# Performance work log

Hardware: AMD Instinct MI355X
Metric: run time of the kernel (lower is better)

## Reference

```python
import jax, jax.numpy as jnp
import numpy as np

U_COUNT = 100000
I_COUNT = 50000
DIM = 64
N_EDGES = 3200000
BATCH = 16384


def setup_inputs() -> dict:
    key = jax.random.key(0)
    ks = jax.random.split(key, 8)
    user_emb = jax.random.normal(ks[0], (U_COUNT, DIM), dtype=jnp.float32) * 0.01
    item_emb = jax.random.normal(ks[1], (I_COUNT, DIM), dtype=jnp.float32) * 0.01
    edge_vals = jax.random.uniform(ks[2], (N_EDGES,), dtype=jnp.float32)
    edge_user = jax.random.randint(ks[3], (N_EDGES,), 0, U_COUNT, dtype=jnp.int32)
    edge_item = jax.random.randint(ks[4], (N_EDGES,), 0, I_COUNT, dtype=jnp.int32)
    user = jax.random.randint(ks[5], (BATCH,), 0, U_COUNT, dtype=jnp.int32)
    pos_item = jax.random.randint(ks[6], (BATCH,), 0, I_COUNT, dtype=jnp.int32)
    neg_item = jax.random.randint(ks[7], (BATCH,), 0, I_COUNT, dtype=jnp.int32)
    return {"user_emb": user_emb, "item_emb": item_emb, "edge_vals": edge_vals,
            "edge_user": edge_user, "edge_item": edge_item,
            "user": user, "pos_item": pos_item, "neg_item": neg_item}


def reference(user_emb, item_emb, edge_vals, edge_user, edge_item, user, pos_item, neg_item):
    # A is the [U, I] normalized adjacency in COO form (edge_user, edge_item, edge_vals).
    # u = A @ x_items : gather item rows, scale, scatter-add into user segments.
    def spmm_A(x_items):  # [I, D] -> [U, D]
        msgs = edge_vals[:, None] * x_items[edge_item]  # [E, D]
        return jax.ops.segment_sum(msgs, edge_user, num_segments=U_COUNT)

    def spmm_AT(x_users):  # [U, D] -> [I, D]
        msgs = edge_vals[:, None] * x_users[edge_user]  # [E, D]
        return jax.ops.segment_sum(msgs, edge_item, num_segments=I_COUNT)

    u_0, i_0 = user_emb, item_emb
    i_1 = spmm_AT(u_0)
    u_1 = spmm_A(i_0)
    # num_layer == 2 branch
    i_2 = spmm_AT(u_1)
    u_2 = spmm_A(i_1)
    u_fin = (u_0 + u_1 + u_2) / 3
    i_fin = (i_0 + i_1 + i_2) / 3

    u = u_fin[user]          # [B, D]
    i = i_fin[pos_item]      # [B, D]
    j = i_fin[neg_item]      # [B, D]
    pos_score = jnp.sum(u * i, axis=1, keepdims=True)  # [B, 1]
    neg_score = jnp.sum(u * j, axis=1, keepdims=True)  # [B, 1]
    return (pos_score, neg_score)
```

## Files before the change

kernel.cpp:

```cpp
#include <hip/hip_runtime.h>

#define U_COUNT 100000
#define I_COUNT 50000
#define DIM     64
#define N_EDGES 3200000
#define BATCH   16384
#define N_NODES (U_COUNT + I_COUNT)
#define SCAN_B  256
#define NBLK    ((N_NODES + SCAN_B - 1) / SCAN_B)
#define NPASS   8
#define PRANGE  ((N_NODES + NPASS - 1) / NPASS)


__global__ __launch_bounds__(256) void hist_kernel(
    const int* __restrict__ eu, const int* __restrict__ ei, int* __restrict__ deg)
{
    int e = blockIdx.x * blockDim.x + threadIdx.x;
    if (e >= N_EDGES) return;
    atomicAdd(&deg[eu[e]], 1);
    atomicAdd(&deg[U_COUNT + ei[e]], 1);
}

__global__ __launch_bounds__(SCAN_B) void scan1_kernel(
    const int* __restrict__ deg, int* __restrict__ blocksum)
{
    __shared__ int s[SCAN_B];
    int t = threadIdx.x, g = blockIdx.x * SCAN_B + t;
    s[t] = (g < N_NODES) ? deg[g] : 0;
    __syncthreads();
    for (int off = SCAN_B / 2; off > 0; off >>= 1) {
        if (t < off) s[t] += s[t + off];
        __syncthreads();
    }
    if (t == 0) blocksum[blockIdx.x] = s[0];
}

__global__ __launch_bounds__(1024) void scan2_kernel(
    const int* __restrict__ blocksum, int* __restrict__ blockoff)
{
    __shared__ int s[1024];
    int t = threadIdx.x;
    s[t] = (t < NBLK) ? blocksum[t] : 0;
    __syncthreads();
    for (int off = 1; off < 1024; off <<= 1) {
        int v = (t >= off) ? s[t - off] : 0;
        __syncthreads();
        s[t] += v;
        __syncthreads();
    }
    if (t < NBLK) blockoff[t] = s[t] - blocksum[t];
}

__global__ __launch_bounds__(SCAN_B) void scan3_kernel(
    const int* __restrict__ deg, const int* __restrict__ blockoff,
    int* __restrict__ row_start, int* __restrict__ cursor)
{
    __shared__ int s[SCAN_B];
    int t = threadIdx.x, g = blockIdx.x * SCAN_B + t;
    int v = (g < N_NODES) ? deg[g] : 0;
    s[t] = v;
    __syncthreads();
    for (int off = 1; off < SCAN_B; off <<= 1) {
        int w = (t >= off) ? s[t - off] : 0;
        __syncthreads();
        s[t] += w;
        __syncthreads();
    }
    if (g < N_NODES) {
        int excl = s[t] - v + blockoff[blockIdx.x];
        row_start[g] = excl;
        cursor[g]    = excl;
    }
}

__global__ __launch_bounds__(256) void scatter_pass(
    const int* __restrict__ eu, const int* __restrict__ ei, const float* __restrict__ ev,
    int* __restrict__ cursor, int2* __restrict__ csr, int lo, int hi)
{
    int e = blockIdx.x * blockDim.x + threadIdx.x;
    if (e >= N_EDGES) return;
    int u  = eu[e];
    int it = ei[e];
    int nu = u;
    int ni = U_COUNT + it;
    bool wu = (nu >= lo) & (nu < hi);
    bool wi = (ni >= lo) & (ni < hi);
    if (wu | wi) {
        float v = ev[e];
        if (wu) {
            int p = atomicAdd(&cursor[nu], 1);
            csr[p] = make_int2(it, __float_as_int(v));
        }
        if (wi) {
            int p = atomicAdd(&cursor[ni], 1);
            csr[p] = make_int2(u, __float_as_int(v));
        }
    }
}

__global__ __launch_bounds__(256) void spmm_pull_all(
    const int2* __restrict__ list,
    const int*  __restrict__ rstart,
    const int*  __restrict__ rend,
    const float* __restrict__ user_emb,
    const float* __restrict__ item_emb,
    float* __restrict__ u1, float* __restrict__ i1)
{
    int tid = blockIdx.x * blockDim.x + threadIdx.x;
    int r = tid >> 6;
    int d = tid & 63;
    if (r >= N_NODES) return;
    r = __builtin_amdgcn_readfirstlane(r);
    const float* src;
    float* dst;
    if (r < U_COUNT) { src = item_emb; dst = &u1[(size_t)r * DIM]; }
    else             { src = user_emb; dst = &i1[(size_t)(r - U_COUNT) * DIM]; }
    int k   = rstart[r];
    int end = rend[r];
    float acc = 0.f;
    for (; k + 4 <= end; k += 4) {
        int2 e0 = list[k], e1 = list[k + 1], e2 = list[k + 2], e3 = list[k + 3];
        acc = fmaf(__int_as_float(e0.y), src[(size_t)e0.x * DIM + d], acc);
        acc = fmaf(__int_as_float(e1.y), src[(size_t)e1.x * DIM + d], acc);
        acc = fmaf(__int_as_float(e2.y), src[(size_t)e2.x * DIM + d], acc);
        acc = fmaf(__int_as_float(e3.y), src[(size_t)e3.x * DIM + d], acc);
    }
    for (; k < end; ++k) {
        int2 e0 = list[k];
        acc = fmaf(__int_as_float(e0.y), src[(size_t)e0.x * DIM + d], acc);
    }
    dst[d] = acc;
}

__global__ __launch_bounds__(256) void score_fused(
    const float* __restrict__ u0, const float* __restrict__ i0,
    const float* __restrict__ u1, const float* __restrict__ i1,
    const int2* __restrict__ csr,
    const int* __restrict__ urs, const int* __restrict__ ure,
    const int* __restrict__ irs, const int* __restrict__ ire,
    const int* __restrict__ user, const int* __restrict__ pos, const int* __restrict__ neg,
    float* __restrict__ out)
{
    int tid = blockIdx.x * blockDim.x + threadIdx.x;
    int b = tid >> 6;
    int d = tid & 63;
    if (b >= BATCH) return;
    int uu = user[b], pp = pos[b], nn = neg[b];

    float u2v = 0.f;
    for (int k = urs[uu], e = ure[uu]; k < e; ++k) {
        int2 ed = csr[k];
        u2v = fmaf(__int_as_float(ed.y), i1[(size_t)ed.x * DIM + d], u2v);
    }
    float i2p = 0.f;
    for (int k = irs[pp], e = ire[pp]; k < e; ++k) {
        int2 ed = csr[k];
        i2p = fmaf(__int_as_float(ed.y), u1[(size_t)ed.x * DIM + d], i2p);
    }
    float i2n = 0.f;
    for (int k = irs[nn], e = ire[nn]; k < e; ++k) {
        int2 ed = csr[k];
        i2n = fmaf(__int_as_float(ed.y), u1[(size_t)ed.x * DIM + d], i2n);
    }

    const float third = 1.0f / 3.0f;
    float uf = (u0[(size_t)uu * DIM + d] + u1[(size_t)uu * DIM + d] + u2v) * third;
    float pf = (i0[(size_t)pp * DIM + d] + i1[(size_t)pp * DIM + d] + i2p) * third;
    float nf = (i0[(size_t)nn * DIM + d] + i1[(size_t)nn * DIM + d] + i2n) * third;
    float ps = uf * pf;
    float ns = uf * nf;
    #pragma unroll
    for (int off = 32; off > 0; off >>= 1) {
        ps += __shfl_xor(ps, off, 64);
        ns += __shfl_xor(ns, off, 64);
    }
    if (d == 0) {
        out[b]         = ps;
        out[BATCH + b] = ns;
    }
}

__global__ __launch_bounds__(256) void spmm_both(
    const float* __restrict__ x_user, const float* __restrict__ x_item,
    const float* __restrict__ edge_vals,
    const int* __restrict__ edge_user, const int* __restrict__ edge_item,
    float* __restrict__ out_item, float* __restrict__ out_user)
{
    long long tid = (long long)blockIdx.x * blockDim.x + threadIdx.x;
    int e = (int)(tid >> 6);
    int d = (int)(tid & 63);
    if (e >= N_EDGES) return;
    int   u  = edge_user[e];
    int   it = edge_item[e];
    float v  = edge_vals[e];
    float xu = x_user[(long long)u  * DIM + d];
    float xi = x_item[(long long)it * DIM + d];
    atomicAdd(&out_item[(long long)it * DIM + d], v * xu);
    atomicAdd(&out_user[(long long)u  * DIM + d], v * xi);
}

__global__ __launch_bounds__(256) void score_kernel(
    const float* __restrict__ u0, const float* __restrict__ u1, const float* __restrict__ u2,
    const float* __restrict__ i0, const float* __restrict__ i1, const float* __restrict__ i2,
    const int* __restrict__ user, const int* __restrict__ pos, const int* __restrict__ neg,
    float* __restrict__ out)
{
    int tid = blockIdx.x * blockDim.x + threadIdx.x;
    int b = tid >> 6;
    int d = tid & 63;
    if (b >= BATCH) return;
    int uu = user[b], pp = pos[b], nn = neg[b];
    const float third = 1.0f / 3.0f;
    float uf = (u0[(size_t)uu * DIM + d] + u1[(size_t)uu * DIM + d] + u2[(size_t)uu * DIM + d]) * third;
    float pf = (i0[(size_t)pp * DIM + d] + i1[(size_t)pp * DIM + d] + i2[(size_t)pp * DIM + d]) * third;
    float nf = (i0[(size_t)nn * DIM + d] + i1[(size_t)nn * DIM + d] + i2[(size_t)nn * DIM + d]) * third;
    float ps = uf * pf;
    float ns = uf * nf;
    #pragma unroll
    for (int off = 32; off > 0; off >>= 1) {
        ps += __shfl_xor(ps, off, 64);
        ns += __shfl_xor(ns, off, 64);
    }
    if (d == 0) {
        out[b]         = ps;
        out[BATCH + b] = ns;
    }
}

extern "C" void kernel_launch(void* const* d_in, const int* in_sizes, int n_in,
                              void* d_out, int out_size, void* d_ws, size_t ws_size,
                              hipStream_t stream) {
    const float* user_emb  = (const float*)d_in[0];
    const float* item_emb  = (const float*)d_in[1];
    const float* edge_vals = (const float*)d_in[2];
    const int*   edge_user = (const int*)d_in[3];
    const int*   edge_item = (const int*)d_in[4];
    const int*   user      = (const int*)d_in[5];
    const int*   pos_item  = (const int*)d_in[6];
    const int*   neg_item  = (const int*)d_in[7];
    float* out = (float*)d_out;

    char* ws = (char*)d_ws;
    size_t off = 0;
    auto carve = [&](size_t bytes) { char* p = ws + off; off = (off + bytes + 255) & ~(size_t)255; return p; };
    int*  deg       = (int*) carve((size_t)N_NODES * 4);
    int*  row_start = (int*) carve((size_t)N_NODES * 4);
    int*  cursor    = (int*) carve((size_t)N_NODES * 4);
    int*  blocksum  = (int*) carve((size_t)NBLK * 4);
    int*  blockoff  = (int*) carve((size_t)NBLK * 4);
    int2* csr       = (int2*)carve((size_t)2 * N_EDGES * 8);
    float* i1       = (float*)carve((size_t)I_COUNT * DIM * 4);
    float* u1       = (float*)carve((size_t)U_COUNT * DIM * 4);
    size_t need_fast = off;

    int edge_blocks = (N_EDGES + 255) / 256;

    if (ws_size >= need_fast) {
        hipMemsetAsync(deg, 0, (size_t)N_NODES * 4, stream);

        hist_kernel <<<edge_blocks, 256, 0, stream>>>(edge_user, edge_item, deg);
        scan1_kernel<<<NBLK, SCAN_B, 0, stream>>>(deg, blocksum);
        scan2_kernel<<<1, 1024, 0, stream>>>(blocksum, blockoff);
        scan3_kernel<<<NBLK, SCAN_B, 0, stream>>>(deg, blockoff, row_start, cursor);

        for (int p = 0; p < NPASS; ++p) {
            int lo = p * PRANGE;
            int hi = (p == NPASS - 1) ? N_NODES : lo + PRANGE;
            scatter_pass<<<edge_blocks, 256, 0, stream>>>(edge_user, edge_item, edge_vals,
                                                          cursor, csr, lo, hi);
        }

        spmm_pull_all<<<(N_NODES * 64) / 256, 256, 0, stream>>>(
            csr, row_start, cursor, user_emb, item_emb, u1, i1);

        score_fused<<<(BATCH * 64) / 256, 256, 0, stream>>>(
            user_emb, item_emb, u1, i1, csr,
            row_start, cursor, row_start + U_COUNT, cursor + U_COUNT,
            user, pos_item, neg_item, out);
    } else {
        float* fi1 = (float*)d_ws;
        float* fu1 = fi1 + (size_t)I_COUNT * DIM;
        float* fi2 = fu1 + (size_t)U_COUNT * DIM;
        float* fu2 = fi2 + (size_t)I_COUNT * DIM;
        size_t accum_bytes = ((size_t)I_COUNT + (size_t)U_COUNT) * DIM * 2 * sizeof(float);
        hipMemsetAsync(d_ws, 0, accum_bytes, stream);

        int eb64 = (N_EDGES + 3) / 4;
        spmm_both<<<eb64, 256, 0, stream>>>(user_emb, item_emb, edge_vals,
                                            edge_user, edge_item, fi1, fu1);
        spmm_both<<<eb64, 256, 0, stream>>>(fu1, fi1, edge_vals,
                                            edge_user, edge_item, fi2, fu2);
        score_kernel<<<(BATCH * 64) / 256, 256, 0, stream>>>(user_emb, fu1, fu2,
                                                             item_emb, fi1, fi2,
                                                             user, pos_item, neg_item, out);
    }
}
```

Measured before the change: 1.149 ms.

## Replace global-atomic degree histogram with multi-pass LDS-privatized packed histograms

The degree histogram now runs in five range passes. Each block keeps private shared-memory bins that pack two 16-bit counters per word, and the blocks write partial histograms into the unused CSR buffer. A merge kernel then sums the partials into deg. The aim is to avoid 6.4M contended global atomics and the memset, at the cost of reading the edge arrays five times, a 60KB LDS allocation per block that limits occupancy, and a merge pass over 128 partials.

```diff
diff --git a/kernel.cpp b/kernel.cpp
--- a/kernel.cpp
+++ b/kernel.cpp
@@ -11,14 +11,58 @@
 #define NPASS   8
 #define PRANGE  ((N_NODES + NPASS - 1) / NPASS)
 
-
-__global__ __launch_bounds__(256) void hist_kernel(
-    const int* __restrict__ eu, const int* __restrict__ ei, int* __restrict__ deg)
-{
-    int e = blockIdx.x * blockDim.x + threadIdx.x;
-    if (e >= N_EDGES) return;
-    atomicAdd(&deg[eu[e]], 1);
-    atomicAdd(&deg[U_COUNT + ei[e]], 1);
+#define HPASS   5
+#define HRANGE  (N_NODES / HPASS)
+#define HWORDS  (HRANGE / 2)
+#define HB      128
+
+__global__ __launch_bounds__(256) void hist_lds(
+    const int4* __restrict__ eu4, const int4* __restrict__ ei4,
+    unsigned int* __restrict__ partial,
+    int lo)
+{
+    __shared__ unsigned int bins[HWORDS];
+    for (int w = threadIdx.x; w < HWORDS; w += 256) bins[w] = 0;
+    __syncthreads();
+
+    const int nvec = N_EDGES / 4;
+    for (int v = blockIdx.x * 256 + threadIdx.x; v < nvec; v += HB * 256) {
+        int4 u  = eu4[v];
+        int4 it = ei4[v];
+        int n;
+        n = u.x - lo;              if ((unsigned)n < (unsigned)HRANGE) atomicAdd(&bins[n >> 1], (n & 1) ? 0x10000u : 1u);
+        n = u.y - lo;              if ((unsigned)n < (unsigned)HRANGE) atomicAdd(&bins[n >> 1], (n & 1) ? 0x10000u : 1u);
+        n = u.z - lo;              if ((unsigned)n < (unsigned)HRANGE) atomicAdd(&bins[n >> 1], (n & 1) ? 0x10000u : 1u);
+        n = u.w - lo;              if ((unsigned)n < (unsigned)HRANGE) atomicAdd(&bins[n >> 1], (n & 1) ? 0x10000u : 1u);
+        n = U_COUNT + it.x - lo;   if ((unsigned)n < (unsigned)HRANGE) atomicAdd(&bins[n >> 1], (n & 1) ? 0x10000u : 1u);
+        n = U_COUNT + it.y - lo;   if ((unsigned)n < (unsigned)HRANGE) atomicAdd(&bins[n >> 1], (n & 1) ? 0x10000u : 1u);
+        n = U_COUNT + it.z - lo;   if ((unsigned)n < (unsigned)HRANGE) atomicAdd(&bins[n >> 1], (n & 1) ? 0x10000u : 1u);
+        n = U_COUNT + it.w - lo;   if ((unsigned)n < (unsigned)HRANGE) atomicAdd(&bins[n >> 1], (n & 1) ? 0x10000u : 1u);
+    }
+    __syncthreads();
+
+    unsigned int* dst = partial + (size_t)blockIdx.x * HWORDS;
+    for (int w = threadIdx.x; w < HWORDS; w += 256) dst[w] = bins[w];
+}
+
+__global__ __launch_bounds__(256) void merge_deg(
+    const unsigned int* __restrict__ partial,
+    int* __restrict__ deg)
+{
+    int idx = blockIdx.x * blockDim.x + threadIdx.x;
+    if (idx >= HPASS * HWORDS) return;
+    int p = idx / HWORDS;
+    int w = idx - p * HWORDS;
+    const unsigned int* base = partial + (size_t)p * HB * HWORDS + w;
+    unsigned int lo_s = 0, hi_s = 0;
+    for (int b = 0; b < HB; ++b) {
+        unsigned int v = base[(size_t)b * HWORDS];
+        lo_s += v & 0xFFFFu;
+        hi_s += v >> 16;
+    }
+    int node = p * HRANGE + 2 * w;
+    deg[node]     = (int)lo_s;
+    deg[node + 1] = (int)hi_s;
 }
 
 __global__ __launch_bounds__(SCAN_B) void scan1_kernel(
@@ -253,12 +297,17 @@
     float* u1       = (float*)carve((size_t)U_COUNT * DIM * 4);
     size_t need_fast = off;
 
+    unsigned int* partial = (unsigned int*)csr;
+
     int edge_blocks = (N_EDGES + 255) / 256;
 
     if (ws_size >= need_fast) {
-        hipMemsetAsync(deg, 0, (size_t)N_NODES * 4, stream);
-
-        hist_kernel <<<edge_blocks, 256, 0, stream>>>(edge_user, edge_item, deg);
+        for (int p = 0; p < HPASS; ++p) {
+            hist_lds<<<HB, 256, 0, stream>>>((const int4*)edge_user, (const int4*)edge_item,
+                                             partial + (size_t)p * HB * HWORDS, p * HRANGE);
+        }
+        merge_deg<<<(HPASS * HWORDS + 255) / 256, 256, 0, stream>>>(partial, deg);
+
         scan1_kernel<<<NBLK, SCAN_B, 0, stream>>>(deg, blocksum);
         scan2_kernel<<<1, 1024, 0, stream>>>(blocksum, blockoff);
         scan3_kernel<<<NBLK, SCAN_B, 0, stream>>>(deg, blockoff, row_start, cursor);
```

After: 981.7 us. 1.17x faster.
